# Kernel tuning notes

Measured on AMD Instinct MI355X. Metric: run time of the kernel, lower is better.

Reference implementation:

```python
import jax, jax.numpy as jnp
import numpy as np

B, T, N, H, NHEADS, DFF, DEMO = 128, 128, 76, 64, 4, 256, 12

def _lin(x, W, b):
    # torch Linear: y = x @ W.T + b, W is [out, in]
    return jnp.matmul(x, W.T) + b

def _layernorm(x, g, b, eps=1e-7):
    mu = x.mean(-1, keepdims=True)
    var = ((x - mu) ** 2).mean(-1, keepdims=True)
    return (x - mu) / jnp.sqrt(var + eps) * g + b

def _gru_all_features(X, Wih, Whh, bih, bhh):
    # X: [B,T,N]; Wih: [N,3H] (input_size=1); Whh: [N,3H,H]; biases [N,3H]
    # PyTorch gate order: r, z, n. Returns H_seq [B,N,T,H].
    Bsz, Tlen, Nf = X.shape
    Hd = Whh.shape[-1]
    h0 = jnp.zeros((Bsz, Nf, Hd), X.dtype)
    def step(h, x_t):  # h [B,N,H], x_t [B,N]
        ih = x_t[:, :, None] * Wih[None] + bih[None]            # [B,N,3H]
        hh = jnp.einsum('bnh,ngh->bng', h, Whh) + bhh[None]     # [B,N,3H]
        r = jax.nn.sigmoid(ih[..., :Hd] + hh[..., :Hd])
        z = jax.nn.sigmoid(ih[..., Hd:2 * Hd] + hh[..., Hd:2 * Hd])
        n = jnp.tanh(ih[..., 2 * Hd:] + r * hh[..., 2 * Hd:])
        h_new = (1.0 - z) * n + z * h
        return h_new, h_new
    _, Hs = jax.lax.scan(step, h0, jnp.moveaxis(X, 1, 0))       # [T,B,N,H]
    return jnp.transpose(Hs, (1, 2, 0, 3))                      # [B,N,T,H]

def _time_attention(Hs, Wt, bt, Wx, bx, rate):
    # Hs [B,N,T,H]; Wt/Wx [N,H,H]; bt/bx [N,H]; rate [N]
    Tlen = Hs.shape[2]
    q = jnp.einsum('bnh,nkh->bnk', Hs[:, :, -1, :], Wt) + bt[None]          # [B,N,H]
    K = jnp.einsum('bnth,nkh->bntk', Hs, Wx) + bx[None, :, None, :]         # [B,N,T,H]
    dot = jnp.einsum('bnk,bntk->bnt', q, K)                                 # [B,N,T]
    tdecay = jnp.arange(1, Tlen + 1, dtype=Hs.dtype)                        # [1..T]
    ds = jax.nn.sigmoid(dot)
    denom = jax.nn.sigmoid(rate)[None, :, None] * jnp.log(2.72 + (1.0 - ds)) * tdecay
    denom = jnp.maximum(denom, 1e-6)
    e = jax.nn.relu(ds / denom)
    alpha = jax.nn.softmax(e, axis=-1)
    return jnp.einsum('bnt,bnth->bnh', alpha, Hs)                           # [B,N,H]

def _mha_decov(x, Wq, bq, Wk, bk, Wv, bv, Wo, bo, n_heads):
    Bsz, L, Dm = x.shape
    dk = Dm // n_heads
    def split(t):
        return t.reshape(Bsz, L, n_heads, dk).transpose(0, 2, 1, 3)
    q, k, v = split(_lin(x, Wq, bq)), split(_lin(x, Wk, bk)), split(_lin(x, Wv, bv))
    scores = jnp.matmul(q, k.transpose(0, 1, 3, 2)) / (dk ** 0.5)
    attn = jax.nn.softmax(scores, axis=-1)
    head = jnp.matmul(attn, v)                                              # [B,h,L,dk]
    merged = head.transpose(0, 2, 1, 3).reshape(Bsz, L, Dm)
    out = _lin(merged, Wo, bo)
    U = merged.reshape(Bsz * L, Dm)
    U = U - U.mean(0, keepdims=True)
    C = (U.T @ U) / max(Bsz * L, 1)
    decov = 0.5 * ((C ** 2).sum() - (jnp.diag(C) ** 2).sum())
    return out, decov

def setup_inputs():
    key = jax.random.key(0)
    ks = jax.random.split(key, 32)
    s = 0.08
    def rn(k, shape):
        return jax.random.normal(k, shape, jnp.float32) * s
    inp = {
        'X': jax.random.normal(ks[0], (B, T, N), jnp.float32),
        'D': jax.random.normal(ks[1], (B, DEMO), jnp.float32),
        'gru_Wih': rn(ks[2], (N, 3 * H)),
        'gru_Whh': rn(ks[3], (N, 3 * H, H)),
        'gru_bih': jnp.zeros((N, 3 * H), jnp.float32),
        'gru_bhh': jnp.zeros((N, 3 * H), jnp.float32),
        'att_Wt': rn(ks[4], (N, H, H)),
        'att_bt': jnp.zeros((N, H), jnp.float32),
        'att_Wx': rn(ks[5], (N, H, H)),
        'att_bx': jnp.zeros((N, H), jnp.float32),
        'att_rate': jnp.zeros((N,), jnp.float32),
        'demo_W': rn(ks[6], (H, DEMO)),
        'demo_b': jnp.zeros((H,), jnp.float32),
        'mh_Wq': rn(ks[7], (H, H)), 'mh_bq': rn(ks[8], (H,)),
        'mh_Wk': rn(ks[9], (H, H)), 'mh_bk': rn(ks[10], (H,)),
        'mh_Wv': rn(ks[11], (H, H)), 'mh_bv': rn(ks[12], (H,)),
        'mh_Wo': rn(ks[13], (H, H)), 'mh_bo': rn(ks[14], (H,)),
        'ln1_g': jnp.ones((H,), jnp.float32), 'ln1_b': jnp.zeros((H,), jnp.float32),
        'ffn_W1': rn(ks[15], (DFF, H)), 'ffn_b1': rn(ks[16], (DFF,)),
        'ffn_W2': rn(ks[17], (H, DFF)), 'ffn_b2': rn(ks[18], (H,)),
        'ln2_g': jnp.ones((H,), jnp.float32), 'ln2_b': jnp.zeros((H,), jnp.float32),
        'fa_Wq': rn(ks[19], (H, H)), 'fa_bq': rn(ks[20], (H,)),
        'fa_Wk': rn(ks[21], (H, H)), 'fa_bk': rn(ks[22], (H,)),
        'fa_Wv': rn(ks[23], (H, H)), 'fa_bv': rn(ks[24], (H,)),
        'fa_Wout': rn(ks[25], (1, H)), 'fa_bout': rn(ks[26], (1,)),
        'out0_W': rn(ks[27], (H, H)), 'out0_b': jnp.zeros((H,), jnp.float32),
        'out1_W': rn(ks[28], (1, H)), 'out1_b': jnp.zeros((1,), jnp.float32),
    }
    return inp

def _forward(X, D, gru_Wih, gru_Whh, gru_bih, gru_bhh, att_Wt, att_bt, att_Wx, att_bx,
             att_rate, demo_W, demo_b, mh_Wq, mh_bq, mh_Wk, mh_bk, mh_Wv, mh_bv, mh_Wo,
             mh_bo, ln1_g, ln1_b, ffn_W1, ffn_b1, ffn_W2, ffn_b2, ln2_g, ln2_b,
             fa_Wq, fa_bq, fa_Wk, fa_bk, fa_Wv, fa_bv, fa_Wout, fa_bout,
             out0_W, out0_b, out1_W, out1_b):
    Hs = _gru_all_features(X, gru_Wih, gru_Whh, gru_bih, gru_bhh)   # [B,N,T,H]
    F_dyn = _time_attention(Hs, att_Wt, att_bt, att_Wx, att_bx, att_rate)  # [B,N,H]
    f_demo = jnp.tanh(_lin(D, demo_W, demo_b))[:, None, :]
    F_in = jnp.concatenate([F_dyn, f_demo], axis=1)                 # [B,N+1,H]
    _, decov = _mha_decov(F_in, mh_Wq, mh_bq, mh_Wk, mh_bk, mh_Wv, mh_bv, mh_Wo, mh_bo, NHEADS)
    attn_out, _ = _mha_decov(_layernorm(F_in, ln1_g, ln1_b), mh_Wq, mh_bq, mh_Wk, mh_bk,
                             mh_Wv, mh_bv, mh_Wo, mh_bo, NHEADS)
    Y = F_in + attn_out
    z = _layernorm(Y, ln2_g, ln2_b)
    Z = Y + _lin(jax.nn.relu(_lin(z, ffn_W1, ffn_b1)), ffn_W2, ffn_b2)
    # FinalAttentionQKV
    Q = _lin(Z, fa_Wq, fa_bq)
    K = _lin(Z, fa_Wk, fa_bk)
    V = _lin(Z, fa_Wv, fa_bv)
    scores = _lin(Q * K, fa_Wout, fa_bout)[..., 0]                  # [B,L]
    alpha = jax.nn.softmax(scores, axis=1)
    s = jnp.einsum('bl,blh->bh', alpha, V)
    h = jax.nn.relu(_lin(s, out0_W, out0_b))
    y_prob = jax.nn.sigmoid(_lin(h, out1_W, out1_b))
    return y_prob, decov

def reference(X, D, gru_Wih, gru_Whh, gru_bih, gru_bhh, att_Wt, att_bt, att_Wx, att_bx,
              att_rate, demo_W, demo_b, mh_Wq, mh_bq, mh_Wk, mh_bk, mh_Wv, mh_bv, mh_Wo,
              mh_bo, ln1_g, ln1_b, ffn_W1, ffn_b1, ffn_W2, ffn_b2, ln2_g, ln2_b,
              fa_Wq, fa_bq, fa_Wk, fa_bk, fa_Wv, fa_bv, fa_Wout, fa_bout,
              out0_W, out0_b, out1_W, out1_b):
    return _forward(X, D, gru_Wih, gru_Whh, gru_bih, gru_bhh, att_Wt, att_bt, att_Wx,
                    att_bx, att_rate, demo_W, demo_b, mh_Wq, mh_bq, mh_Wk, mh_bk, mh_Wv,
                    mh_bv, mh_Wo, mh_bo, ln1_g, ln1_b, ffn_W1, ffn_b1, ffn_W2, ffn_b2,
                    ln2_g, ln2_b, fa_Wq, fa_bq, fa_Wk, fa_bk, fa_Wv, fa_bv, fa_Wout,
                    fa_bout, out0_W, out0_b, out1_W, out1_b)
```

## Files before the change

kernel.cpp:

```cpp
#include <hip/hip_runtime.h>
#include <math.h>

#define B_ 128
#define T_ 128
#define NF 76
#define HD 64
#define LQ 77

typedef __attribute__((ext_vector_type(8))) short short8v;
typedef __attribute__((ext_vector_type(4))) short short4v;
typedef __attribute__((ext_vector_type(4))) float f32x4;

__device__ __forceinline__ float frcp(float x) { return __builtin_amdgcn_rcpf(x); }
__device__ __forceinline__ float sigmf(float x) { return frcp(1.0f + __expf(-x)); }
__device__ __forceinline__ float tanh_fast(float x) { return 2.0f * frcp(1.0f + __expf(-2.0f * x)) - 1.0f; }
__device__ __forceinline__ short tobf(float x) {
    unsigned u = __float_as_uint(x);
    u += 0x7FFF + ((u >> 16) & 1);
    return (short)(u >> 16);
}
__device__ __forceinline__ float bflo(unsigned u) { return __uint_as_float(u << 16); }
__device__ __forceinline__ float bfhi(unsigned u) { return __uint_as_float(u & 0xffff0000u); }

__global__ __launch_bounds__(256) void k_gru0(
    const float* __restrict__ X, const float* __restrict__ Wih,
    const float* __restrict__ Whh, const float* __restrict__ bih,
    const float* __restrict__ bhh,
    const float* __restrict__ Wt, const float* __restrict__ bt,
    const float* __restrict__ Wx, const float* __restrict__ bx,
    short* __restrict__ Hsg, float* __restrict__ qxg, float* __restrict__ qbg)
{
    __shared__ short As[2][16 * 72];
    __shared__ float xs[16 * 129];
    __shared__ float q1[16 * 65];
    __shared__ float q2[16 * 65];

    const int nf = blockIdx.y;
    const int chunk = blockIdx.x;
    const int cbase = chunk * 16;
    const int tid = threadIdx.x;
    const int w = tid >> 6;
    const int lane = tid & 63;
    const int col = lane & 15;
    const int quad = lane >> 4;

    for (int i = tid; i < 16 * T_; i += 256) {
        int b = i >> 7, t = i & 127;
        xs[b * 129 + t] = X[((size_t)(cbase + b) * T_ + t) * NF + nf];
    }

    short8v bfr[3][2];
    const float* wbase = Whh + (size_t)nf * 12288;
#pragma unroll
    for (int g3 = 0; g3 < 3; ++g3)
#pragma unroll
        for (int k2 = 0; k2 < 2; ++k2) {
            int g = 64 * g3 + 16 * w + col;
            const float* src = wbase + g * 64 + 32 * k2 + quad * 8;
            float4 f0 = *(const float4*)src;
            float4 f1 = *(const float4*)(src + 4);
            short8v fr;
            fr[0] = tobf(f0.x); fr[1] = tobf(f0.y); fr[2] = tobf(f0.z); fr[3] = tobf(f0.w);
            fr[4] = tobf(f1.x); fr[5] = tobf(f1.y); fr[6] = tobf(f1.z); fr[7] = tobf(f1.w);
            bfr[g3][k2] = fr;
        }

    const int c = 16 * w + col;
    const int base = nf * 192;
    const float wr = Wih[base + c], wz = Wih[base + 64 + c], wn = Wih[base + 128 + c];
    const float br = bih[base + c] + bhh[base + c];
    const float bz = bih[base + 64 + c] + bhh[base + 64 + c];
    const float bnn = bih[base + 128 + c], bhn = bhh[base + 128 + c];

    for (int i = tid; i < 16 * 72; i += 256) As[0][i] = 0;
    float hold[4];
#pragma unroll
    for (int r = 0; r < 4; ++r) hold[r] = 0.0f;
    __syncthreads();

    const int crow = tid >> 4, cs = tid & 15;

    for (int t = 0; t < T_; ++t) {
        const int rb = t & 1;
        const int wb = 1 - rb;
        short8v A0 = *(const short8v*)&As[rb][col * 72 + quad * 8];
        short8v A1 = *(const short8v*)&As[rb][col * 72 + 32 + quad * 8];

        f32x4 acc[3];
#pragma unroll
        for (int g3 = 0; g3 < 3; ++g3) {
            f32x4 a = {0.0f, 0.0f, 0.0f, 0.0f};
            a = __builtin_amdgcn_mfma_f32_16x16x32_bf16(A0, bfr[g3][0], a, 0, 0, 0);
            a = __builtin_amdgcn_mfma_f32_16x16x32_bf16(A1, bfr[g3][1], a, 0, 0, 0);
            acc[g3] = a;
        }

#pragma unroll
        for (int r = 0; r < 4; ++r) {
            float xv = xs[(quad * 4 + r) * 129 + t];
            float rr = sigmf(xv * wr + br + acc[0][r]);
            float zz = sigmf(xv * wz + bz + acc[1][r]);
            float nn = tanh_fast(xv * wn + bnn + rr * (acc[2][r] + bhn));
            hold[r] = (1.0f - zz) * nn + zz * hold[r];
        }

#pragma unroll
        for (int r = 0; r < 4; ++r)
            As[wb][(quad * 4 + r) * 72 + c] = tobf(hold[r]);
        __syncthreads();
        {
            uint2 pk = *(const uint2*)&As[wb][crow * 72 + cs * 4];
            size_t go = (((size_t)nf * 128 + cbase + crow) * 128 + t) * 64 + cs * 4;
            *(uint2*)(Hsg + go) = pk;
        }
    }

#pragma unroll
    for (int r = 0; r < 4; ++r)
        q1[(quad * 4 + r) * 65 + c] = hold[r];
    __syncthreads();
    for (int o = tid; o < 16 * 64; o += 256) {
        int b = o >> 6, k = o & 63;
        const float* wrow = Wt + ((size_t)nf * 64 + k) * 64;
        float a = bt[nf * 64 + k];
#pragma unroll 8
        for (int h = 0; h < 64; h += 4) {
            float4 wv = *(const float4*)&wrow[h];
            a += q1[b * 65 + h] * wv.x + q1[b * 65 + h + 1] * wv.y
               + q1[b * 65 + h + 2] * wv.z + q1[b * 65 + h + 3] * wv.w;
        }
        q2[b * 65 + k] = a;
    }
    __syncthreads();
    for (int o = tid; o < 16 * 64; o += 256) {
        int b = o >> 6, h = o & 63;
        float a = 0.0f;
#pragma unroll 8
        for (int k = 0; k < 64; ++k)
            a += q2[b * 65 + k] * Wx[((size_t)nf * 64 + k) * 64 + h];
        qxg[((size_t)nf * 128 + cbase + b) * 64 + h] = a;
    }
    for (int b = tid; b < 16; b += 256) {
        float a = 0.0f;
        for (int k = 0; k < 64; ++k) a += q2[b * 65 + k] * bx[nf * 64 + k];
        qbg[nf * 128 + cbase + b] = a;
    }
}

__global__ __launch_bounds__(128) void k_att(
    const short* __restrict__ Hsg, const float* __restrict__ qxg,
    const float* __restrict__ qbg, const float* __restrict__ rate,
    const float* __restrict__ D, const float* __restrict__ dW,
    const float* __restrict__ db, float* __restrict__ Sz,
    float* __restrict__ Fin)
{
    const int nf = blockIdx.x, b = blockIdx.y;
    const int tid = threadIdx.x;

    if (nf == NF) {
        if (tid < 64) {
            float acc = db[tid];
            for (int j = 0; j < 12; ++j) acc += D[b * 12 + j] * dW[tid * 12 + j];
            Fin[((size_t)b * LQ + 76) * HD + tid] = tanh_fast(acc);
        }
        int s0 = b * 33;
        for (int k = tid; k < 33; k += 128) {
            int idx = s0 + k;
            if (idx < 4161) Sz[idx] = 0.0f;
        }
        return;
    }

    __shared__ float wsum[128 * 69];
    __shared__ float wl[128];
    __shared__ float qxl[64];
    __shared__ float pn[2][68];
    __shared__ float pd[2];
    if (tid < 64) qxl[tid] = qxg[((size_t)nf * 128 + b) * 64 + tid];
    const float qb = qbg[nf * 128 + b];
    const float sigr = sigmf(rate[nf]);

    uint4 rv[8];
    const uint4* src = (const uint4*)(Hsg + (((size_t)nf * 128 + b) * 128 + tid) * 64);
#pragma unroll
    for (int k = 0; k < 8; ++k) rv[k] = src[k];
    __syncthreads();

    float a = qb;
#pragma unroll
    for (int k = 0; k < 8; ++k) {
        a += bflo(rv[k].x) * qxl[k * 8 + 0] + bfhi(rv[k].x) * qxl[k * 8 + 1]
           + bflo(rv[k].y) * qxl[k * 8 + 2] + bfhi(rv[k].y) * qxl[k * 8 + 3]
           + bflo(rv[k].z) * qxl[k * 8 + 4] + bfhi(rv[k].z) * qxl[k * 8 + 5]
           + bflo(rv[k].w) * qxl[k * 8 + 6] + bfhi(rv[k].w) * qxl[k * 8 + 7];
    }
    float ds = sigmf(a);
    float dn = fmaxf(sigr * __logf(2.72f + (1.0f - ds)) * (float)(tid + 1), 1e-6f);
    float e = fmaxf(ds * frcp(dn), 0.0f);
    float w = __expf(e);
    wl[tid] = w;
#pragma unroll
    for (int k = 0; k < 8; ++k) {
        float* d = &wsum[tid * 69 + k * 8];
        d[0] = w * bflo(rv[k].x); d[1] = w * bfhi(rv[k].x);
        d[2] = w * bflo(rv[k].y); d[3] = w * bfhi(rv[k].y);
        d[4] = w * bflo(rv[k].z); d[5] = w * bfhi(rv[k].z);
        d[6] = w * bflo(rv[k].w); d[7] = w * bfhi(rv[k].w);
    }
    __syncthreads();
    {
        int ch = tid & 63, half = tid >> 6;
        float acc = 0.0f, den = 0.0f;
        int t0 = half * 64;
        for (int t = t0; t < t0 + 64; ++t) {
            acc += wsum[t * 69 + ch];
            den += wl[t];
        }
        pn[half][ch] = acc;
        if (ch == 0) pd[half] = den;
    }
    __syncthreads();
    if (tid < 64) {
        float num = pn[0][tid] + pn[1][tid];
        float den = pd[0] + pd[1];
        Fin[((size_t)b * LQ + nf) * HD + tid] = num * frcp(den);
    }
}

__global__ __launch_bounds__(256) void k_mha2(
    const float* __restrict__ Fin,
    const float* __restrict__ Wq, const float* __restrict__ bq,
    const float* __restrict__ Wk, const float* __restrict__ bk,
    const float* __restrict__ Wv, const float* __restrict__ bv,
    const float* __restrict__ g1, const float* __restrict__ b1,
    float* __restrict__ M1, float* __restrict__ M2)
{
    __shared__ float xl[LQ * 68];
    __shared__ float qh[LQ * 20], kh[LQ * 20], vh[LQ * 20];
    float (*os)[17] = (float (*)[17])xl;
    const int b = blockIdx.x, hd = blockIdx.y, v = blockIdx.z;
    const int tid = threadIdx.x;
    const float* xsrc = Fin + (size_t)b * LQ * HD;

    for (int idx = tid; idx < LQ * HD; idx += 256)
        xl[(idx >> 6) * 68 + (idx & 63)] = xsrc[idx];
    __syncthreads();
    if (v == 1) {
        if (tid < LQ) {
            float mu = 0.0f;
            for (int h = 0; h < 64; ++h) mu += xl[tid * 68 + h];
            mu *= (1.0f / 64.0f);
            float var = 0.0f;
            for (int h = 0; h < 64; ++h) { float d = xl[tid * 68 + h] - mu; var += d * d; }
            var *= (1.0f / 64.0f);
            float rs = rsqrtf(var + 1e-7f);
            for (int h = 0; h < 64; ++h)
                xl[tid * 68 + h] = (xl[tid * 68 + h] - mu) * rs * g1[h] + b1[h];
        }
        __syncthreads();
    }

    for (int idx = tid; idx < LQ * 16; idx += 256) {
        int l = idx >> 4, d = idx & 15, ch = hd * 16 + d;
        float aq = bq[ch], ak = bk[ch], av = bv[ch];
        const float4* wq = (const float4*)(Wq + ch * 64);
        const float4* wk = (const float4*)(Wk + ch * 64);
        const float4* wv = (const float4*)(Wv + ch * 64);
        const float4* xr = (const float4*)&xl[l * 68];
#pragma unroll 4
        for (int c4 = 0; c4 < 16; ++c4) {
            float4 xv = xr[c4];
            float4 a = wq[c4], bb = wk[c4], cc = wv[c4];
            aq += xv.x * a.x + xv.y * a.y + xv.z * a.z + xv.w * a.w;
            ak += xv.x * bb.x + xv.y * bb.y + xv.z * bb.z + xv.w * bb.w;
            av += xv.x * cc.x + xv.y * cc.y + xv.z * cc.z + xv.w * cc.w;
        }
        qh[l * 20 + d] = aq; kh[l * 20 + d] = ak; vh[l * 20 + d] = av;
    }
    __syncthreads();

    if (tid < 231) {
        int l = tid % 77, third = tid / 77;
        float4 qf0 = *(const float4*)&qh[l * 20 + 0];
        float4 qf1 = *(const float4*)&qh[l * 20 + 4];
        float4 qf2 = *(const float4*)&qh[l * 20 + 8];
        float4 qf3 = *(const float4*)&qh[l * 20 + 12];
        int j0 = third * 26;
        int j1 = (third == 2) ? LQ : j0 + 26;
        float o[16];
#pragma unroll
        for (int d = 0; d < 16; ++d) o[d] = 0.0f;
        float ss = 0.0f;
        for (int j = j0; j < j1; ++j) {
            const float4* kp = (const float4*)&kh[j * 20];
            float4 k0 = kp[0], k1 = kp[1], k2 = kp[2], k3 = kp[3];
            float sc = qf0.x * k0.x + qf0.y * k0.y + qf0.z * k0.z + qf0.w * k0.w
                     + qf1.x * k1.x + qf1.y * k1.y + qf1.z * k1.z + qf1.w * k1.w
                     + qf2.x * k2.x + qf2.y * k2.y + qf2.z * k2.z + qf2.w * k2.w
                     + qf3.x * k3.x + qf3.y * k3.y + qf3.z * k3.z + qf3.w * k3.w;
            float p = __expf(sc * 0.25f);
            ss += p;
            const float4* vp = (const float4*)&vh[j * 20];
            float4 v0 = vp[0], v1 = vp[1], v2 = vp[2], v3 = vp[3];
            o[0] += p * v0.x; o[1] += p * v0.y; o[2] += p * v0.z; o[3] += p * v0.w;
            o[4] += p * v1.x; o[5] += p * v1.y; o[6] += p * v1.z; o[7] += p * v1.w;
            o[8] += p * v2.x; o[9] += p * v2.y; o[10] += p * v2.z; o[11] += p * v2.w;
            o[12] += p * v3.x; o[13] += p * v3.y; o[14] += p * v3.z; o[15] += p * v3.w;
        }
#pragma unroll
        for (int d = 0; d < 16; ++d) os[tid][d] = o[d];
        os[tid][16] = ss;
    }
    __syncthreads();
    if (tid < LQ) {
        float inv = frcp(os[tid][16] + os[77 + tid][16] + os[154 + tid][16]);
        float* Mout = (v == 1) ? M2 : M1;
#pragma unroll
        for (int d = 0; d < 16; ++d)
            Mout[((size_t)b * LQ + tid) * HD + hd * 16 + d]
                = (os[tid][d] + os[77 + tid][d] + os[154 + tid][d]) * inv;
    }
}

__global__ __launch_bounds__(256) void k_zff(
    const float* __restrict__ Fin, float* __restrict__ M2,
    const float* __restrict__ Wo, const float* __restrict__ bo,
    const float* __restrict__ g2, const float* __restrict__ b2,
    const float* __restrict__ W1, const float* __restrict__ bb1,
    const float* __restrict__ W2, const float* __restrict__ bb2,
    const float* __restrict__ faWq, const float* __restrict__ fabq,
    const float* __restrict__ faWk, const float* __restrict__ fabk,
    const float* __restrict__ faWv, const float* __restrict__ fabv,
    const float* __restrict__ faWout, const float* __restrict__ fabout,
    float* __restrict__ scout)
{
    __shared__ float m2l[16 * 68];
    __shared__ float yl[16 * 68];
    __shared__ float zl[16 * 68];
    __shared__ float ul[16 * 260];
    const int tid = threadIdx.x;
    const size_t base = (size_t)blockIdx.x * 16;
    const size_t eb = base * 64;
    const int h = tid & 63, rq = tid >> 6;

    for (int idx = tid; idx < 1024; idx += 256)
        m2l[(idx >> 6) * 68 + (idx & 63)] = M2[eb + idx];
    __syncthreads();

    {
        float acc[4];
#pragma unroll
        for (int rr = 0; rr < 4; ++rr) acc[rr] = bo[h];
        const float4* wo = (const float4*)(Wo + h * 64);
#pragma unroll 4
        for (int c4 = 0; c4 < 16; ++c4) {
            float4 wv = wo[c4];
#pragma unroll
            for (int rr = 0; rr < 4; ++rr) {
                float4 mv = *(const float4*)&m2l[(rq * 4 + rr) * 68 + c4 * 4];
                acc[rr] += mv.x * wv.x + mv.y * wv.y + mv.z * wv.z + mv.w * wv.w;
            }
        }
#pragma unroll
        for (int rr = 0; rr < 4; ++rr) {
            int r = rq * 4 + rr;
            yl[r * 68 + h] = Fin[eb + r * 64 + h] + acc[rr];
        }
    }
    __syncthreads();
    if (tid < 16) {
        float mu = 0.0f;
        for (int c = 0; c < 64; ++c) mu += yl[tid * 68 + c];
        mu *= (1.0f / 64.0f);
        float var = 0.0f;
        for (int c = 0; c < 64; ++c) { float d = yl[tid * 68 + c] - mu; var += d * d; }
        var *= (1.0f / 64.0f);
        float rs = rsqrtf(var + 1e-7f);
        for (int c = 0; c < 64; ++c)
            zl[tid * 68 + c] = (yl[tid * 68 + c] - mu) * rs * g2[c] + b2[c];
    }
    __syncthreads();

    {
        const int f = tid;
        float acc[16];
#pragma unroll
        for (int r = 0; r < 16; ++r) acc[r] = bb1[f];
        const float4* w1r = (const float4*)(W1 + f * 64);
#pragma unroll
        for (int c = 0; c < 4; ++c) {
            float4 w0 = w1r[c * 4 + 0], w1 = w1r[c * 4 + 1];
            float4 w2 = w1r[c * 4 + 2], w3 = w1r[c * 4 + 3];
#pragma unroll
            for (int r = 0; r < 16; ++r) {
                const float4* zr = (const float4*)&zl[r * 68 + c * 16];
                float4 z0 = zr[0], z1 = zr[1], z2 = zr[2], z3 = zr[3];
                acc[r] += z0.x * w0.x + z0.y * w0.y + z0.z * w0.z + z0.w * w0.w
                        + z1.x * w1.x + z1.y * w1.y + z1.z * w1.z + z1.w * w1.w
                        + z2.x * w2.x + z2.y * w2.y + z2.z * w2.z + z2.w * w2.w
                        + z3.x * w3.x + z3.y * w3.y + z3.z * w3.z + z3.w * w3.w;
            }
        }
#pragma unroll
        for (int r = 0; r < 16; ++r) ul[r * 260 + f] = fmaxf(acc[r], 0.0f);
    }
    __syncthreads();
    {
        float acc[4];
#pragma unroll
        for (int rr = 0; rr < 4; ++rr) acc[rr] = bb2[h];
        const float4* w2r = (const float4*)(W2 + h * 256);
#pragma unroll 4
        for (int c = 0; c < 16; ++c) {
            float4 w0 = w2r[c * 4 + 0], w1 = w2r[c * 4 + 1];
            float4 w2 = w2r[c * 4 + 2], w3 = w2r[c * 4 + 3];
#pragma unroll
            for (int rr = 0; rr < 4; ++rr) {
                const float4* ur = (const float4*)&ul[(rq * 4 + rr) * 260 + c * 16];
                float4 u0 = ur[0], u1 = ur[1], u2 = ur[2], u3 = ur[3];
                acc[rr] += u0.x * w0.x + u0.y * w0.y + u0.z * w0.z + u0.w * w0.w
                         + u1.x * w1.x + u1.y * w1.y + u1.z * w1.z + u1.w * w1.w
                         + u2.x * w2.x + u2.y * w2.y + u2.z * w2.z + u2.w * w2.w
                         + u3.x * w3.x + u3.y * w3.y + u3.z * w3.z + u3.w * w3.w;
            }
        }
#pragma unroll
        for (int rr = 0; rr < 4; ++rr)
            yl[(rq * 4 + rr) * 68 + h] += acc[rr];
    }
    __syncthreads();

    {
        const float4* wq = (const float4*)(faWq + h * 64);
        const float4* wk = (const float4*)(faWk + h * 64);
        const float4* wv = (const float4*)(faWv + h * 64);
        float q[4], k[4], v[4];
#pragma unroll
        for (int rr = 0; rr < 4; ++rr) { q[rr] = fabq[h]; k[rr] = fabk[h]; v[rr] = fabv[h]; }
#pragma unroll 4
        for (int c4 = 0; c4 < 16; ++c4) {
            float4 a = wq[c4], bb = wk[c4], cc = wv[c4];
#pragma unroll
            for (int rr = 0; rr < 4; ++rr) {
                float4 zv = *(const float4*)&yl[(rq * 4 + rr) * 68 + c4 * 4];
                q[rr] += zv.x * a.x + zv.y * a.y + zv.z * a.z + zv.w * a.w;
                k[rr] += zv.x * bb.x + zv.y * bb.y + zv.z * bb.z + zv.w * bb.w;
                v[rr] += zv.x * cc.x + zv.y * cc.y + zv.z * cc.z + zv.w * cc.w;
            }
        }
        float fw = faWout[h];
#pragma unroll
        for (int rr = 0; rr < 4; ++rr) {
            int r = rq * 4 + rr;
            ul[r * 68 + h] = q[rr] * k[rr] * fw;
            M2[eb + r * 64 + h] = v[rr];
        }
    }
    __syncthreads();
    if (tid < 16) {
        float a = fabout[0];
        for (int c = 0; c < 64; ++c) a += ul[tid * 68 + c];
        scout[base + tid] = a;
    }
}

__global__ __launch_bounds__(256) void k_cov(
    const float* __restrict__ M1, float* __restrict__ S, float* __restrict__ MU,
    unsigned* __restrict__ cnt, float* __restrict__ out)
{
    __shared__ float tile[64 * 64];
    const int tid = threadIdx.x;
    const int ig = tid >> 6, j = tid & 63;
    const int i = blockIdx.x * 4 + ig;
    const int l0 = blockIdx.y * 308;
    float acc = 0.0f, mua = 0.0f;
    for (int c0 = 0; c0 < 308; c0 += 64) {
        int rows = (308 - c0 < 64) ? (308 - c0) : 64;
        __syncthreads();
        const float4* gsrc = (const float4*)(M1 + (size_t)(l0 + c0) * 64);
        for (int idx = tid; idx < rows * 16; idx += 256)
            *(float4*)&tile[idx * 4] = gsrc[idx];
        __syncthreads();
#pragma unroll 4
        for (int l = 0; l < rows; ++l) {
            float v = tile[l * 64 + j];
            acc += tile[l * 64 + i] * v;
            mua += v;
        }
    }
    atomicAdd(&S[i * 64 + j], acc);
    if (blockIdx.x == 0 && ig == 0) atomicAdd(&MU[j], mua);
    __threadfence();
    __syncthreads();
    __shared__ unsigned lastf;
    if (tid == 0) lastf = (atomicAdd(cnt, 1u) == 511u);
    __syncthreads();
    if (lastf) {
        __shared__ float mus[64];
        __shared__ float pa[4], pd[4];
        if (tid < 64) mus[tid] = atomicAdd(&MU[tid], 0.0f);
        __syncthreads();
        const float invM = 1.0f / 9856.0f;
        float asum = 0.0f, dsum = 0.0f;
        for (int idx = tid; idx < 4096; idx += 256) {
            int ii = idx >> 6, jj = idx & 63;
            float c = atomicAdd(&S[idx], 0.0f) * invM - (mus[ii] * invM) * (mus[jj] * invM);
            asum += c * c;
            if (ii == jj) dsum += c * c;
        }
        for (int o = 32; o; o >>= 1) {
            asum += __shfl_xor(asum, o, 64);
            dsum += __shfl_xor(dsum, o, 64);
        }
        if ((tid & 63) == 0) { pa[tid >> 6] = asum; pd[tid >> 6] = dsum; }
        __syncthreads();
        if (tid == 0)
            out[128] = 0.5f * ((pa[0] + pa[1] + pa[2] + pa[3])
                             - (pd[0] + pd[1] + pd[2] + pd[3]));
    }
}

__global__ __launch_bounds__(128) void k_head(
    const float* __restrict__ Vg, const float* __restrict__ scout,
    const float* __restrict__ o0W, const float* __restrict__ o0b,
    const float* __restrict__ o1W, const float* __restrict__ o1b,
    float* __restrict__ out)
{
    __shared__ float sl[LQ + 3];
    __shared__ float pn[2][64];
    __shared__ float sv[64], h1[64];
    __shared__ float red0;
    const int b = blockIdx.x, tid = threadIdx.x;

    if (tid < LQ) sl[tid] = scout[b * LQ + tid];
    __syncthreads();
    if (tid < 64) {
        float v0 = sl[tid];
        float v1 = (tid < LQ - 64) ? sl[tid + 64] : -1e30f;
        float m = fmaxf(v0, v1);
        for (int o = 32; o; o >>= 1) m = fmaxf(m, __shfl_xor(m, o, 64));
        float e0 = __expf(v0 - m);
        float e1 = (tid < LQ - 64) ? __expf(v1 - m) : 0.0f;
        float s = e0 + e1;
        for (int o = 32; o; o >>= 1) s += __shfl_xor(s, o, 64);
        sl[tid] = e0;
        if (tid < LQ - 64) sl[tid + 64] = e1;
        if (tid == 0) red0 = s;
    }
    __syncthreads();
    {
        int h = tid & 63, half = tid >> 6;
        int l0 = half ? 39 : 0, l1 = half ? LQ : 39;
        float acc = 0.0f;
#pragma unroll 4
        for (int l = l0; l < l1; ++l)
            acc += sl[l] * Vg[((size_t)b * LQ + l) * 64 + h];
        pn[half][h] = acc;
    }
    __syncthreads();
    if (tid < 64) sv[tid] = (pn[0][tid] + pn[1][tid]) * frcp(red0);
    __syncthreads();
    if (tid < 64) {
        float acc = o0b[tid];
        const float4* w = (const float4*)(o0W + tid * 64);
#pragma unroll 4
        for (int c4 = 0; c4 < 16; ++c4) {
            float4 wv = w[c4];
            const float4* sp = (const float4*)&sv[c4 * 4];
            float4 s0 = sp[0];
            acc += s0.x * wv.x + s0.y * wv.y + s0.z * wv.z + s0.w * wv.w;
        }
        h1[tid] = fmaxf(acc, 0.0f);
    }
    __syncthreads();
    if (tid < 64) {
        float p = h1[tid] * o1W[tid];
        for (int o = 32; o; o >>= 1) p += __shfl_xor(p, o, 64);
        if (tid == 0) out[b] = sigmf(p + o1b[0]);
    }
}

__global__ void k_demo(const float* __restrict__ D, const float* __restrict__ dW,
                       const float* __restrict__ db, float* __restrict__ Fin)
{
    int b = blockIdx.x, h = threadIdx.x;
    float acc = db[h];
    for (int j = 0; j < 12; ++j) acc += D[b * 12 + j] * dW[h * 12 + j];
    Fin[((size_t)b * LQ + 76) * HD + h] = tanh_fast(acc);
}

__global__ void k_zero(float* __restrict__ p)
{
    for (int i = threadIdx.x; i < 4161; i += 256) p[i] = 0.0f;
}

__global__ __launch_bounds__(128) void k_gru_mfma(
    const float* __restrict__ X, const float* __restrict__ Wih,
    const float* __restrict__ Whh, const float* __restrict__ bih,
    const float* __restrict__ bhh,
    const float* __restrict__ Wt, const float* __restrict__ bt,
    const float* __restrict__ Wx, const float* __restrict__ bx,
    const float* __restrict__ rate, float* __restrict__ Fin)
{
    __shared__ short As[2][16 * 68];
    __shared__ float xs[16 * 129];
    __shared__ float q1[16 * 65];
    __shared__ float q2[16 * 65];
    __shared__ float qbs[16];
    __shared__ float dotw[2][2][16];

    const int nf = blockIdx.y;
    const int cbase = blockIdx.x * 16;
    const int tid = threadIdx.x;
    const int w = tid >> 6;
    const int lane = tid & 63;
    const int col = lane & 15;
    const int quad = lane >> 4;

    for (int i = tid; i < 16 * T_; i += 128) {
        int b = i >> 7, t = i & 127;
        xs[b * 129 + t] = X[((size_t)(cbase + b) * T_ + t) * NF + nf];
    }
    short8v bfr[3][2][2];
    const float* wbase = Whh + (size_t)nf * 12288;
#pragma unroll
    for (int g3 = 0; g3 < 3; ++g3)
#pragma unroll
        for (int s = 0; s < 2; ++s)
#pragma unroll
            for (int k2 = 0; k2 < 2; ++k2) {
                int g = 64 * g3 + 32 * w + 16 * s + col;
                const float* src = wbase + g * 64 + 32 * k2 + quad * 8;
                float4 f0 = *(const float4*)src;
                float4 f1 = *(const float4*)(src + 4);
                short8v fr;
                fr[0] = tobf(f0.x); fr[1] = tobf(f0.y); fr[2] = tobf(f0.z); fr[3] = tobf(f0.w);
                fr[4] = tobf(f1.x); fr[5] = tobf(f1.y); fr[6] = tobf(f1.z); fr[7] = tobf(f1.w);
                bfr[g3][s][k2] = fr;
            }
    float wr[2], wz[2], wn[2], br[2], bz[2], bnn[2], bhn[2];
#pragma unroll
    for (int s = 0; s < 2; ++s) {
        int c = 32 * w + 16 * s + col;
        int base = nf * 192;
        wr[s] = Wih[base + c]; wz[s] = Wih[base + 64 + c]; wn[s] = Wih[base + 128 + c];
        br[s] = bih[base + c] + bhh[base + c];
        bz[s] = bih[base + 64 + c] + bhh[base + 64 + c];
        bnn[s] = bih[base + 128 + c]; bhn[s] = bhh[base + 128 + c];
    }
    const float sigr = sigmf(rate[nf]);
    float hold[2][4], num[2][4], den[4], qxv[2][4], qbv[4];
#pragma unroll
    for (int r = 0; r < 4; ++r) {
        den[r] = 0.0f; qbv[r] = 0.0f;
        num[0][r] = 0.0f; num[1][r] = 0.0f;
        qxv[0][r] = 0.0f; qxv[1][r] = 0.0f;
    }
    for (int pass = 0; pass < 2; ++pass) {
        for (int i = tid; i < 16 * 68; i += 128) As[0][i] = 0;
#pragma unroll
        for (int s = 0; s < 2; ++s)
#pragma unroll
            for (int r = 0; r < 4; ++r) hold[s][r] = 0.0f;
        __syncthreads();
        for (int t = 0; t < T_; ++t) {
            const int rb = t & 1;
            const int wb = 1 - rb;
            const short* ap = &As[rb][col * 68 + quad * 8];
            short4v a0 = *(const short4v*)ap;
            short4v a1 = *(const short4v*)(ap + 4);
            short4v a2 = *(const short4v*)(ap + 32);
            short4v a3 = *(const short4v*)(ap + 36);
            short8v A0 = {a0[0], a0[1], a0[2], a0[3], a1[0], a1[1], a1[2], a1[3]};
            short8v A1 = {a2[0], a2[1], a2[2], a2[3], a3[0], a3[1], a3[2], a3[3]};
            f32x4 acc[3][2];
#pragma unroll
            for (int g3 = 0; g3 < 3; ++g3)
#pragma unroll
                for (int s = 0; s < 2; ++s) {
                    f32x4 a = {0.0f, 0.0f, 0.0f, 0.0f};
                    a = __builtin_amdgcn_mfma_f32_16x16x32_bf16(A0, bfr[g3][s][0], a, 0, 0, 0);
                    a = __builtin_amdgcn_mfma_f32_16x16x32_bf16(A1, bfr[g3][s][1], a, 0, 0, 0);
                    acc[g3][s] = a;
                }
            float xv[4];
#pragma unroll
            for (int r = 0; r < 4; ++r) xv[r] = xs[(quad * 4 + r) * 129 + t];
            float hnew[2][4];
#pragma unroll
            for (int s = 0; s < 2; ++s)
#pragma unroll
                for (int r = 0; r < 4; ++r) {
                    float rr = sigmf(xv[r] * wr[s] + br[s] + acc[0][s][r]);
                    float zz = sigmf(xv[r] * wz[s] + bz[s] + acc[1][s][r]);
                    float nn = tanh_fast(xv[r] * wn[s] + bnn[s] + rr * (acc[2][s][r] + bhn[s]));
                    hnew[s][r] = (1.0f - zz) * nn + zz * hold[s][r];
                    hold[s][r] = hnew[s][r];
                }
#pragma unroll
            for (int s = 0; s < 2; ++s)
#pragma unroll
                for (int r = 0; r < 4; ++r)
                    As[wb][(quad * 4 + r) * 68 + 32 * w + 16 * s + col] = tobf(hnew[s][r]);
            if (pass == 1) {
                float p[4];
#pragma unroll
                for (int r = 0; r < 4; ++r)
                    p[r] = qxv[0][r] * hnew[0][r] + qxv[1][r] * hnew[1][r];
#pragma unroll
                for (int m = 1; m < 16; m <<= 1) {
                    p[0] += __shfl_xor(p[0], m, 64);
                    p[1] += __shfl_xor(p[1], m, 64);
                    p[2] += __shfl_xor(p[2], m, 64);
                    p[3] += __shfl_xor(p[3], m, 64);
                }
                if (col == 0) {
#pragma unroll
                    for (int r = 0; r < 4; ++r) dotw[rb][w][quad * 4 + r] = p[r];
                }
                __syncthreads();
                float tf = (float)(t + 1);
#pragma unroll
                for (int r = 0; r < 4; ++r) {
                    float dot = p[r] + dotw[rb][1 - w][quad * 4 + r] + qbv[r];
                    float ds = sigmf(dot);
                    float dn = fmaxf(sigr * __logf(2.72f + (1.0f - ds)) * tf, 1e-6f);
                    float e = fmaxf(ds * frcp(dn), 0.0f);
                    float wt = __expf(e);
                    den[r] += wt;
                    num[0][r] += wt * hnew[0][r];
                    num[1][r] += wt * hnew[1][r];
                }
            } else {
                __syncthreads();
            }
        }
        if (pass == 0) {
#pragma unroll
            for (int s = 0; s < 2; ++s)
#pragma unroll
                for (int r = 0; r < 4; ++r)
                    q1[(quad * 4 + r) * 65 + 32 * w + 16 * s + col] = hold[s][r];
            __syncthreads();
            for (int o = tid; o < 16 * 64; o += 128) {
                int b = o >> 6, k = o & 63;
                const float* wrow = Wt + ((size_t)nf * 64 + k) * 64;
                float a = bt[nf * 64 + k];
#pragma unroll 8
                for (int h = 0; h < 64; h += 4) {
                    float4 wv = *(const float4*)&wrow[h];
                    a += q1[b * 65 + h] * wv.x + q1[b * 65 + h + 1] * wv.y
                       + q1[b * 65 + h + 2] * wv.z + q1[b * 65 + h + 3] * wv.w;
                }
                q2[b * 65 + k] = a;
            }
            __syncthreads();
            for (int o = tid; o < 16 * 64; o += 128) {
                int b = o >> 6, h = o & 63;
                float a = 0.0f;
#pragma unroll 8
                for (int k = 0; k < 64; ++k)
                    a += q2[b * 65 + k] * Wx[((size_t)nf * 64 + k) * 64 + h];
                q1[b * 65 + h] = a;
            }
            for (int b = tid; b < 16; b += 128) {
                float a = 0.0f;
                for (int k = 0; k < 64; ++k) a += q2[b * 65 + k] * bx[nf * 64 + k];
                qbs[b] = a;
            }
            __syncthreads();
#pragma unroll
            for (int r = 0; r < 4; ++r) {
                qbv[r] = qbs[quad * 4 + r];
#pragma unroll
                for (int s = 0; s < 2; ++s)
                    qxv[s][r] = q1[(quad * 4 + r) * 65 + 32 * w + 16 * s + col];
                den[r] = 0.0f; num[0][r] = 0.0f; num[1][r] = 0.0f;
            }
            __syncthreads();
        }
    }
#pragma unroll
    for (int s = 0; s < 2; ++s)
#pragma unroll
        for (int r = 0; r < 4; ++r) {
            int b = cbase + quad * 4 + r;
            int c = 32 * w + 16 * s + col;
            Fin[((size_t)b * LQ + nf) * HD + c] = num[s][r] * frcp(den[r]);
        }
}

extern "C" void kernel_launch(void* const* d_in, const int* in_sizes, int n_in,
                              void* d_out, int out_size, void* d_ws, size_t ws_size,
                              hipStream_t stream)
{
    (void)in_sizes; (void)n_in; (void)out_size;
    const float* X     = (const float*)d_in[0];
    const float* D     = (const float*)d_in[1];
    const float* gWih  = (const float*)d_in[2];
    const float* gWhh  = (const float*)d_in[3];
    const float* gbih  = (const float*)d_in[4];
    const float* gbhh  = (const float*)d_in[5];
    const float* aWt   = (const float*)d_in[6];
    const float* abt   = (const float*)d_in[7];
    const float* aWx   = (const float*)d_in[8];
    const float* abx   = (const float*)d_in[9];
    const float* arate = (const float*)d_in[10];
    const float* dW    = (const float*)d_in[11];
    const float* db    = (const float*)d_in[12];
    const float* mWq   = (const float*)d_in[13]; const float* mbq = (const float*)d_in[14];
    const float* mWk   = (const float*)d_in[15]; const float* mbk = (const float*)d_in[16];
    const float* mWv   = (const float*)d_in[17]; const float* mbv = (const float*)d_in[18];
    const float* mWo   = (const float*)d_in[19]; const float* mbo = (const float*)d_in[20];
    const float* l1g   = (const float*)d_in[21]; const float* l1b = (const float*)d_in[22];
    const float* fW1   = (const float*)d_in[23]; const float* fb1 = (const float*)d_in[24];
    const float* fW2   = (const float*)d_in[25]; const float* fb2 = (const float*)d_in[26];
    const float* l2g   = (const float*)d_in[27]; const float* l2b = (const float*)d_in[28];
    const float* faWq  = (const float*)d_in[29]; const float* fabq = (const float*)d_in[30];
    const float* faWk  = (const float*)d_in[31]; const float* fabk = (const float*)d_in[32];
    const float* faWv  = (const float*)d_in[33]; const float* fabv = (const float*)d_in[34];
    const float* faWo  = (const float*)d_in[35]; const float* fabo = (const float*)d_in[36];
    const float* o0W   = (const float*)d_in[37]; const float* o0b  = (const float*)d_in[38];
    const float* o1W   = (const float*)d_in[39]; const float* o1b  = (const float*)d_in[40];

    float* ws  = (float*)d_ws;
    float* Fin = ws;
    float* M1  = Fin + 630784;
    float* M2  = M1  + 630784;
    float* S   = M2  + 630784;
    float* MU  = S   + 4096;
    unsigned* cnt = (unsigned*)(MU + 64);
    float* qxg = MU + 128;
    float* scout = qxg + 622592;
    short* Hsg = (short*)(scout + 9856);
    const size_t need = (size_t)(630784 * 3 + 4096 + 128 + 622592 + 9856) * 4
                        + (size_t)79691776 * 2;
    float* outp = (float*)d_out;
    float* qbg = scout;

    if (ws_size >= need) {
        k_gru0<<<dim3(8, NF), 256, 0, stream>>>(X, gWih, gWhh, gbih, gbhh,
                                                aWt, abt, aWx, abx, Hsg, qxg, qbg);
        k_att<<<dim3(NF + 1, B_), 128, 0, stream>>>(Hsg, qxg, qbg, arate,
                                                    D, dW, db, S, Fin);
    } else {
        k_gru_mfma<<<dim3(8, NF), 128, 0, stream>>>(X, gWih, gWhh, gbih, gbhh,
                                                    aWt, abt, aWx, abx, arate, Fin);
        k_demo<<<B_, 64, 0, stream>>>(D, dW, db, Fin);
        k_zero<<<1, 256, 0, stream>>>(S);
    }
    k_mha2<<<dim3(B_, 4, 2), 256, 0, stream>>>(Fin, mWq, mbq, mWk, mbk, mWv, mbv,
                                               l1g, l1b, M1, M2);
    k_zff<<<616, 256, 0, stream>>>(Fin, M2, mWo, mbo, l2g, l2b,
                                   fW1, fb1, fW2, fb2,
                                   faWq, fabq, faWk, fabk, faWv, fabv,
                                   faWo, fabo, scout);
    k_cov<<<dim3(16, 32), 256, 0, stream>>>(M1, S, MU, cnt, outp);
    k_head<<<B_, 128, 0, stream>>>(M2, scout, o0W, o0b, o1W, o1b, outp);
}
```

Measured before the change: 525.6 us.

## Batch GRU hidden-state stores over 8 timesteps and fold exp scaling into weights

The GRU recurrence kernel now keeps an 8-slot ring of hidden-state tiles in LDS and writes them to global memory once every 8 steps as 16-byte vector stores, replacing the small per-step 8-byte stores. It also pre-scales the recurrent and input weights and biases by log2(e) (doubled for the candidate gate) so the gates can use exp2 directly, and rewrites tanh as 2*sigmoid-1. The LDS row stride changes from 72 to 68, so A-fragment loads are split into 4-element pieces. The flush adds an extra barrier every 8 steps, and scaling the weights before bf16 rounding slightly changes the rounding.

Measured after the change: 519.6 us. About the same (-1.1%).

```diff
diff --git a/kernel.cpp b/kernel.cpp
--- a/kernel.cpp
+++ b/kernel.cpp
@@ -13,6 +13,7 @@
 
 __device__ __forceinline__ float frcp(float x) { return __builtin_amdgcn_rcpf(x); }
 __device__ __forceinline__ float sigmf(float x) { return frcp(1.0f + __expf(-x)); }
+__device__ __forceinline__ float sigm2(float x) { return frcp(1.0f + __builtin_amdgcn_exp2f(-x)); }
 __device__ __forceinline__ float tanh_fast(float x) { return 2.0f * frcp(1.0f + __expf(-2.0f * x)) - 1.0f; }
 __device__ __forceinline__ short tobf(float x) {
     unsigned u = __float_as_uint(x);
@@ -30,7 +31,7 @@
     const float* __restrict__ Wx, const float* __restrict__ bx,
     short* __restrict__ Hsg, float* __restrict__ qxg, float* __restrict__ qbg)
 {
-    __shared__ short As[2][16 * 72];
+    __shared__ short As[8][16 * 68];
     __shared__ float xs[16 * 129];
     __shared__ float q1[16 * 65];
     __shared__ float q2[16 * 65];
@@ -44,6 +45,9 @@
     const int col = lane & 15;
     const int quad = lane >> 4;
 
+    const float S1 = 1.44269504f;
+    const float S2 = 2.88539008f;
+
     for (int i = tid; i < 16 * T_; i += 256) {
         int b = i >> 7, t = i & 127;
         xs[b * 129 + t] = X[((size_t)(cbase + b) * T_ + t) * NF + nf];
@@ -52,7 +56,8 @@
     short8v bfr[3][2];
     const float* wbase = Whh + (size_t)nf * 12288;
 #pragma unroll
-    for (int g3 = 0; g3 < 3; ++g3)
+    for (int g3 = 0; g3 < 3; ++g3) {
+        const float sc = (g3 == 2) ? S2 : S1;
 #pragma unroll
         for (int k2 = 0; k2 < 2; ++k2) {
             int g = 64 * g3 + 16 * w + col;
@@ -60,31 +65,40 @@
             float4 f0 = *(const float4*)src;
             float4 f1 = *(const float4*)(src + 4);
             short8v fr;
-            fr[0] = tobf(f0.x); fr[1] = tobf(f0.y); fr[2] = tobf(f0.z); fr[3] = tobf(f0.w);
-            fr[4] = tobf(f1.x); fr[5] = tobf(f1.y); fr[6] = tobf(f1.z); fr[7] = tobf(f1.w);
+            fr[0] = tobf(f0.x * sc); fr[1] = tobf(f0.y * sc);
+            fr[2] = tobf(f0.z * sc); fr[3] = tobf(f0.w * sc);
+            fr[4] = tobf(f1.x * sc); fr[5] = tobf(f1.y * sc);
+            fr[6] = tobf(f1.z * sc); fr[7] = tobf(f1.w * sc);
             bfr[g3][k2] = fr;
         }
+    }
 
     const int c = 16 * w + col;
     const int base = nf * 192;
-    const float wr = Wih[base + c], wz = Wih[base + 64 + c], wn = Wih[base + 128 + c];
-    const float br = bih[base + c] + bhh[base + c];
-    const float bz = bih[base + 64 + c] + bhh[base + 64 + c];
-    const float bnn = bih[base + 128 + c], bhn = bhh[base + 128 + c];
-
-    for (int i = tid; i < 16 * 72; i += 256) As[0][i] = 0;
+    const float wr = Wih[base + c] * S1;
+    const float wz = Wih[base + 64 + c] * S1;
+    const float wn = Wih[base + 128 + c] * S2;
+    const float br = (bih[base + c] + bhh[base + c]) * S1;
+    const float bz = (bih[base + 64 + c] + bhh[base + 64 + c]) * S1;
+    const float bnn = bih[base + 128 + c] * S2;
+    const float bhn = bhh[base + 128 + c] * S2;
+
+    for (int i = tid; i < 16 * 68; i += 256) As[7][i] = 0;
     float hold[4];
 #pragma unroll
     for (int r = 0; r < 4; ++r) hold[r] = 0.0f;
     __syncthreads();
 
-    const int crow = tid >> 4, cs = tid & 15;
-
     for (int t = 0; t < T_; ++t) {
-        const int rb = t & 1;
-        const int wb = 1 - rb;
-        short8v A0 = *(const short8v*)&As[rb][col * 72 + quad * 8];
-        short8v A1 = *(const short8v*)&As[rb][col * 72 + 32 + quad * 8];
+        const int rb = (t + 7) & 7;
+        const int wb = t & 7;
+        const short* ap = &As[rb][col * 68 + quad * 8];
+        short4v a0 = *(const short4v*)ap;
+        short4v a1 = *(const short4v*)(ap + 4);
+        short4v a2 = *(const short4v*)(ap + 32);
+        short4v a3 = *(const short4v*)(ap + 36);
+        short8v A0 = {a0[0], a0[1], a0[2], a0[3], a1[0], a1[1], a1[2], a1[3]};
+        short8v A1 = {a2[0], a2[1], a2[2], a2[3], a3[0], a3[1], a3[2], a3[3]};
 
         f32x4 acc[3];
 #pragma unroll
@@ -98,20 +112,35 @@
 #pragma unroll
         for (int r = 0; r < 4; ++r) {
             float xv = xs[(quad * 4 + r) * 129 + t];
-            float rr = sigmf(xv * wr + br + acc[0][r]);
-            float zz = sigmf(xv * wz + bz + acc[1][r]);
-            float nn = tanh_fast(xv * wn + bnn + rr * (acc[2][r] + bhn));
-            hold[r] = (1.0f - zz) * nn + zz * hold[r];
+            float rr = sigm2(xv * wr + br + acc[0][r]);
+            float zz = sigm2(xv * wz + bz + acc[1][r]);
+            float nn = 2.0f * sigm2(xv * wn + bnn + rr * (acc[2][r] + bhn)) - 1.0f;
+            hold[r] = nn + zz * (hold[r] - nn);
         }
 
 #pragma unroll
         for (int r = 0; r < 4; ++r)
-            As[wb][(quad * 4 + r) * 72 + c] = tobf(hold[r]);
+            As[wb][(quad * 4 + r) * 68 + c] = tobf(hold[r]);
         __syncthreads();
-        {
-            uint2 pk = *(const uint2*)&As[wb][crow * 72 + cs * 4];
-            size_t go = (((size_t)nf * 128 + cbase + crow) * 128 + t) * 64 + cs * 4;
-            *(uint2*)(Hsg + go) = pk;
+
+        if ((t & 7) == 7) {
+            const int oct = tid & 7, bb = (tid >> 3) & 15, k0 = tid >> 7;
+            short4v r0[4], r1[4];
+#pragma unroll
+            for (int s = 0; s < 4; ++s) {
+                const short* p = &As[k0 + 2 * s][bb * 68 + oct * 8];
+                r0[s] = *(const short4v*)p;
+                r1[s] = *(const short4v*)(p + 4);
+            }
+            __syncthreads();
+            const size_t gbase =
+                (((size_t)nf * 128 + cbase + bb) * 128 + (t - 7)) * 64 + oct * 8;
+#pragma unroll
+            for (int s = 0; s < 4; ++s) {
+                short8v v = {r0[s][0], r0[s][1], r0[s][2], r0[s][3],
+                             r1[s][0], r1[s][1], r1[s][2], r1[s][3]};
+                *(short8v*)(Hsg + gbase + (size_t)(k0 + 2 * s) * 64) = v;
+            }
         }
     }
 
```
